# Kernel tuning notes

Measured on AMD Instinct MI355X. Metric: run time of the kernel, lower is better.

The kernel has to match this reference:

```python
import jax, jax.numpy as jnp
import numpy as np

USER_COUNT = 100000
ITEM_COUNT = 100000
DIM = 64
B = 1024
NPOS = 10
NTOP = 50
CLAMP = 40.0
EPS = 1e-05


def setup_inputs() -> dict:
    key = jax.random.key(0)
    k1, k2, k3, k4, k5 = jax.random.split(key, 5)
    user_emb = jax.random.normal(k1, (USER_COUNT, DIM), dtype=jnp.float32) * 0.01
    item_emb = jax.random.normal(k2, (ITEM_COUNT, DIM), dtype=jnp.float32) * 0.01
    batch_user = jax.random.randint(k3, (B,), 0, USER_COUNT)
    pos_items = jax.random.randint(k4, (B, NPOS), 0, ITEM_COUNT)
    top_items = jax.random.randint(k5, (B, NTOP), 0, ITEM_COUNT)
    batch_user_mask = jnp.zeros((B, ITEM_COUNT), dtype=jnp.float32)
    return {
        "user_emb": user_emb,
        "item_emb": item_emb,
        "batch_user": batch_user,
        "pos_items": pos_items,
        "top_items": top_items,
        "batch_user_mask": batch_user_mask,
        "is_final": 1,
    }


def _overall_loss(mat, pos_items, top_items, mask):
    # tops: scores at pos+top indices, [B, NPOS+NTOP]
    tops = jnp.take_along_axis(mat, jnp.concatenate([pos_items, top_items], -1), axis=1)
    tops_els = (jnp.exp(mat) * (1.0 - mask)).sum(1, keepdims=True)  # [B,1]
    els = tops_els - jnp.exp(jnp.take_along_axis(mat, top_items, axis=1)).sum(1, keepdims=True)
    above = tops.reshape(-1, 1)
    below = jnp.broadcast_to(els, (els.shape[0], tops.shape[1])).reshape(-1, 1) + jnp.exp(above)
    below = jnp.log(jnp.clip(below, EPS))
    return -(above - below).sum()


def _rank_loss(mat, pos_items, top_items, mask):
    S_pos = jnp.take_along_axis(mat, pos_items, axis=1)                       # [B,NPOS]
    S_top = jnp.take_along_axis(mat, top_items[:, : NTOP // 2], axis=1)       # [B,NTOP/2]
    exp_masked_sum = (jnp.exp(mat) * (1.0 - mask)).sum(1, keepdims=True)      # [B,1]
    below2 = exp_masked_sum - jnp.exp(S_top).sum(1, keepdims=True)
    above_pos = S_pos.sum(1, keepdims=True)
    above_top = S_top.sum(1, keepdims=True)
    below_pos = jnp.cumsum(jnp.exp(jnp.flip(S_pos, -1)), axis=1)
    below_top = jnp.cumsum(jnp.exp(jnp.flip(S_top, -1)), axis=1)
    below_pos = jnp.log(jnp.clip(below_pos + below2, EPS)).sum(1, keepdims=True)
    below_top = jnp.log(jnp.clip(below_top + below2, EPS)).sum(1, keepdims=True)
    pos_KD_loss = -(above_pos - below_pos).sum()
    S_top_sub = jnp.take_along_axis(mat, top_items[:, : NTOP // 10], axis=1)  # [B,NTOP/10]
    below2_sub = exp_masked_sum - jnp.exp(S_top_sub).sum(1, keepdims=True)
    above_top_sub = S_top_sub.sum(1, keepdims=True)
    below_top_sub = jnp.cumsum(jnp.exp(jnp.flip(S_top_sub, -1)), axis=1)
    below_top_sub = jnp.log(jnp.clip(below_top_sub + below2_sub, EPS)).sum(1, keepdims=True)
    top_KD_loss = -(above_top - below_top).sum() - (above_top_sub - below_top_sub).sum()
    return pos_KD_loss + top_KD_loss / 2


def reference(user_emb, item_emb, batch_user, pos_items, top_items, batch_user_mask, is_final):
    u = user_emb[batch_user]                                  # [B, DIM]
    mat = jnp.clip(u @ item_emb.T, -CLAMP, CLAMP)             # [B, ITEM_COUNT]
    if is_final:
        return _rank_loss(mat, pos_items, top_items, batch_user_mask)
    return _overall_loss(mat, pos_items, top_items, batch_user_mask)
```

## Files before the change

kernel.cpp:

```cpp
#include <hip/hip_runtime.h>
#include <cstddef>
#include <cstdint>

#define USER_COUNT_C 100000
#define ITEM_COUNT_C 100000
#define DIM_C 64
#define B_C 1024
#define NPOS_C 10
#define NTOP_C 50
#define CLAMP_C 40.0f
#define EPS_C 1e-5f

#define NGROUPS 6250
#define NCHUNKS 3125
#define GX 48
#define GY 16

using bf16x8 = __attribute__((ext_vector_type(8))) short;
using f32x4  = __attribute__((ext_vector_type(4))) float;

__global__ void zero_ws_kernel(float* __restrict__ ws) {
    ws[threadIdx.x] = 0.0f;
}

__device__ inline short f2bf(float x) {
    uint32_t b = __float_as_uint(x);
    uint32_t r = (b + 0x7fffu + ((b >> 16) & 1u)) >> 16;
    return (short)r;
}

__device__ inline bf16x8 cvt8(const float* __restrict__ p) {
    float4 v0 = *(const float4*)p;
    float4 v1 = *(const float4*)(p + 4);
    bf16x8 r;
    r[0] = f2bf(v0.x); r[1] = f2bf(v0.y); r[2] = f2bf(v0.z); r[3] = f2bf(v0.w);
    r[4] = f2bf(v1.x); r[5] = f2bf(v1.y); r[6] = f2bf(v1.z); r[7] = f2bf(v1.w);
    return r;
}

__global__ __launch_bounds__(256) void prep_items_kernel(
    const float* __restrict__ item_emb, short* __restrict__ item_bf16) {
    const int t = blockIdx.x * 256 + threadIdx.x;
    const int n16 = t & 15;
    const int q   = (t >> 4) & 3;
    const int h   = (t >> 6) & 1;
    const int g   = t >> 7;
    const int i   = g * 16 + n16;
    bf16x8 v = cvt8(item_emb + (size_t)i * DIM_C + h * 32 + q * 8);
    *(bf16x8*)(item_bf16 + (((size_t)g * 2 + h) * 4 + q) * 128 + n16 * 8) = v;
}

__global__ __launch_bounds__(256, 3) void expsum_mfma5_kernel(
    const float* __restrict__ user_emb,
    const short* __restrict__ item_bf16,
    const int*   __restrict__ batch_user,
    const float* __restrict__ mask,
    float*       __restrict__ exp_sum)
{
    const int tid  = threadIdx.x;
    const int wave = tid >> 6;
    const int lane = tid & 63;
    const int n16  = lane & 15;
    const int quad = lane >> 4;
    const int uBase = blockIdx.y * 64;

    bf16x8 b0[4], b1[4];
    #pragma unroll
    for (int j = 0; j < 4; ++j) {
        const int uidx = batch_user[uBase + j * 16 + n16];
        const float* us = user_emb + (size_t)uidx * DIM_C + quad * 8;
        b0[j] = cvt8(us);
        b1[j] = cvt8(us + 32);
    }

    const float* mbase = mask + (size_t)(uBase + n16) * ITEM_COUNT_C;
    const short* fbase = item_bf16 + quad * 128 + n16 * 8;

    const int c0 = (int)(((long)blockIdx.x * NCHUNKS) / GX);
    const int c1 = (int)(((long)(blockIdx.x + 1) * NCHUNKS) / GX);

    float accE[4] = {0.f, 0.f, 0.f, 0.f};

    for (int c = c0 + wave; c < c1; c += 4) {
        float4 m[4][2];
        #pragma unroll
        for (int j = 0; j < 4; ++j)
            #pragma unroll
            for (int ig = 0; ig < 2; ++ig)
                m[j][ig] = *(const float4*)(mbase + (size_t)j * 16 * ITEM_COUNT_C
                                            + c * 32 + ig * 16 + quad * 4);

        const short* fp = fbase + (size_t)c * 2048;
        const bf16x8 a00 = *(const bf16x8*)fp;
        const bf16x8 a01 = *(const bf16x8*)(fp + 512);
        const bf16x8 a10 = *(const bf16x8*)(fp + 1024);
        const bf16x8 a11 = *(const bf16x8*)(fp + 1536);

        f32x4 acc[2][4];
        #pragma unroll
        for (int j = 0; j < 4; ++j) {
            acc[0][j] = (f32x4){0.f, 0.f, 0.f, 0.f};
            acc[0][j] = __builtin_amdgcn_mfma_f32_16x16x32_bf16(a00, b0[j], acc[0][j], 0, 0, 0);
            acc[0][j] = __builtin_amdgcn_mfma_f32_16x16x32_bf16(a01, b1[j], acc[0][j], 0, 0, 0);
            acc[1][j] = (f32x4){0.f, 0.f, 0.f, 0.f};
            acc[1][j] = __builtin_amdgcn_mfma_f32_16x16x32_bf16(a10, b0[j], acc[1][j], 0, 0, 0);
            acc[1][j] = __builtin_amdgcn_mfma_f32_16x16x32_bf16(a11, b1[j], acc[1][j], 0, 0, 0);
        }

        #pragma unroll
        for (int j = 0; j < 4; ++j)
            #pragma unroll
            for (int ig = 0; ig < 2; ++ig) {
                const float* mp = (const float*)&m[j][ig];
                #pragma unroll
                for (int r = 0; r < 4; ++r) {
                    const float sc = fminf(fmaxf(acc[ig][j][r], -CLAMP_C), CLAMP_C);
                    accE[j] += __expf(sc) * (1.0f - mp[r]);
                }
            }
    }

    #pragma unroll
    for (int j = 0; j < 4; ++j) {
        accE[j] += __shfl_xor(accE[j], 16, 64);
        accE[j] += __shfl_xor(accE[j], 32, 64);
    }
    if (quad == 0) {
        #pragma unroll
        for (int j = 0; j < 4; ++j)
            atomicAdd(&exp_sum[uBase + j * 16 + n16], accE[j]);
    }
}

__global__ __launch_bounds__(256) void expsum_fallback_kernel(
    const float* __restrict__ user_emb,
    const float* __restrict__ item_emb,
    const int*   __restrict__ batch_user,
    const float* __restrict__ mask,
    float*       __restrict__ exp_sum)
{
    const int tid  = threadIdx.x;
    const int wave = tid >> 6;
    const int lane = tid & 63;
    const int n16  = lane & 15;
    const int quad = lane >> 4;
    const int rowBase = blockIdx.y * 64 + wave * 16;

    const int uidx = batch_user[rowBase + n16];
    const float* usrc = user_emb + (size_t)uidx * DIM_C + quad * 8;
    const bf16x8 a0 = cvt8(usrc);
    const bf16x8 a1 = cvt8(usrc + 32);

    float accExp[4] = {0.f, 0.f, 0.f, 0.f};

    for (int t = blockIdx.x; t < NGROUPS / 4; t += 64) {
        const int ibase = t * 64;
        bf16x8 b0[4], b1[4];
        #pragma unroll
        for (int s = 0; s < 4; ++s) {
            const int gi = ibase + s * 16 + n16;
            const float* isrc = item_emb + (size_t)gi * DIM_C + quad * 8;
            b0[s] = cvt8(isrc);
            b1[s] = cvt8(isrc + 32);
        }
        f32x4 acc[4];
        #pragma unroll
        for (int s = 0; s < 4; ++s) {
            acc[s] = (f32x4){0.f, 0.f, 0.f, 0.f};
            acc[s] = __builtin_amdgcn_mfma_f32_16x16x32_bf16(a0, b0[s], acc[s], 0, 0, 0);
            acc[s] = __builtin_amdgcn_mfma_f32_16x16x32_bf16(a1, b1[s], acc[s], 0, 0, 0);
        }
        #pragma unroll
        for (int s = 0; s < 4; ++s)
            #pragma unroll
            for (int reg = 0; reg < 4; ++reg) {
                const int row = rowBase + quad * 4 + reg;
                const float sc = fminf(fmaxf(acc[s][reg], -CLAMP_C), CLAMP_C);
                const float w = 1.0f - mask[(size_t)row * ITEM_COUNT_C + ibase + s * 16 + n16];
                accExp[reg] += __expf(sc) * w;
            }
    }
    #pragma unroll
    for (int off = 1; off < 16; off <<= 1)
        #pragma unroll
        for (int reg = 0; reg < 4; ++reg)
            accExp[reg] += __shfl_xor(accExp[reg], off, 64);
    if (n16 == 0)
        #pragma unroll
        for (int reg = 0; reg < 4; ++reg)
            atomicAdd(&exp_sum[rowBase + quad * 4 + reg], accExp[reg]);
}

__global__ void finalize_kernel(
    const float* __restrict__ user_emb,
    const float* __restrict__ item_emb,
    const int*   __restrict__ batch_user,
    const int*   __restrict__ pos_items,
    const int*   __restrict__ top_items,
    const float* __restrict__ exp_sum,
    const int*   __restrict__ is_final,
    float*       __restrict__ row_loss)
{
    __shared__ float ush[DIM_C];
    __shared__ float s_sh[NPOS_C + NTOP_C];
    const int b = blockIdx.x;
    const int tid = threadIdx.x;
    const int uidx = batch_user[b];
    if (tid < 16)
        *(float4*)&ush[tid * 4] = *(const float4*)(user_emb + (size_t)uidx * DIM_C + tid * 4);
    __syncthreads();

    if (tid < NPOS_C + NTOP_C) {
        const int idx = (tid < NPOS_C) ? pos_items[b * NPOS_C + tid]
                                       : top_items[b * NTOP_C + (tid - NPOS_C)];
        const float* iv = item_emb + (size_t)idx * DIM_C;
        float s = 0.f;
        #pragma unroll
        for (int d4 = 0; d4 < 16; ++d4) {
            const float4 a = *(const float4*)(iv + d4 * 4);
            s += a.x * ush[d4 * 4 + 0] + a.y * ush[d4 * 4 + 1]
               + a.z * ush[d4 * 4 + 2] + a.w * ush[d4 * 4 + 3];
        }
        s_sh[tid] = fminf(fmaxf(s, -CLAMP_C), CLAMP_C);
    }
    __syncthreads();

    if (tid == 0) {
        const float E = exp_sum[b];
        float L;
        if (is_final[0] != 0) {
            float sumExpTop = 0.f, above_top = 0.f;
            for (int i = 0; i < NTOP_C / 2; ++i) {
                const float v = s_sh[NPOS_C + i];
                sumExpTop += __expf(v); above_top += v;
            }
            const float below2 = E - sumExpTop;
            float above_pos = 0.f;
            for (int i = 0; i < NPOS_C; ++i) above_pos += s_sh[i];
            float c = 0.f, below_pos = 0.f;
            for (int i = 0; i < NPOS_C; ++i) {
                c += __expf(s_sh[NPOS_C - 1 - i]);
                below_pos += __logf(fmaxf(c + below2, EPS_C));
            }
            float c2 = 0.f, below_top = 0.f;
            for (int i = 0; i < NTOP_C / 2; ++i) {
                c2 += __expf(s_sh[NPOS_C + NTOP_C / 2 - 1 - i]);
                below_top += __logf(fmaxf(c2 + below2, EPS_C));
            }
            const float pos_KD = below_pos - above_pos;
            float sumExpSub = 0.f, above_sub = 0.f;
            for (int i = 0; i < NTOP_C / 10; ++i) {
                const float v = s_sh[NPOS_C + i];
                sumExpSub += __expf(v); above_sub += v;
            }
            const float below2s = E - sumExpSub;
            float c3 = 0.f, below_sub = 0.f;
            for (int i = 0; i < NTOP_C / 10; ++i) {
                c3 += __expf(s_sh[NPOS_C + NTOP_C / 10 - 1 - i]);
                below_sub += __logf(fmaxf(c3 + below2s, EPS_C));
            }
            const float top_KD = (below_top - above_top) + (below_sub - above_sub);
            L = pos_KD + 0.5f * top_KD;
        } else {
            float sumExpTop = 0.f;
            for (int i = 0; i < NTOP_C; ++i) sumExpTop += __expf(s_sh[NPOS_C + i]);
            const float els = E - sumExpTop;
            L = 0.f;
            for (int j = 0; j < NPOS_C + NTOP_C; ++j) {
                const float a = s_sh[j];
                L += __logf(fmaxf(els + __expf(a), EPS_C)) - a;
            }
        }
        row_loss[b] = L;
    }
}

__global__ void reduce_kernel(const float* __restrict__ rl, float* __restrict__ out) {
    __shared__ float part[16];
    const int tid = threadIdx.x;
    float v = rl[tid];
    #pragma unroll
    for (int off = 32; off > 0; off >>= 1) v += __shfl_down(v, off, 64);
    if ((tid & 63) == 0) part[tid >> 6] = v;
    __syncthreads();
    if (tid == 0) {
        float s = 0.f;
        #pragma unroll
        for (int i = 0; i < 16; ++i) s += part[i];
        out[0] = s;
    }
}

extern "C" void kernel_launch(void* const* d_in, const int* in_sizes, int n_in,
                              void* d_out, int out_size, void* d_ws, size_t ws_size,
                              hipStream_t stream) {
    const float* user_emb   = (const float*)d_in[0];
    const float* item_emb   = (const float*)d_in[1];
    const int*   batch_user = (const int*)d_in[2];
    const int*   pos_items  = (const int*)d_in[3];
    const int*   top_items  = (const int*)d_in[4];
    const float* mask       = (const float*)d_in[5];
    const int*   is_final   = (const int*)d_in[6];
    float* out = (float*)d_out;

    float* exp_sum  = (float*)d_ws;
    float* row_loss = exp_sum + B_C;
    short* item_bf16 = (short*)(row_loss + B_C);
    const size_t need = 2 * B_C * sizeof(float)
                      + (size_t)NGROUPS * 1024 * sizeof(short);

    hipLaunchKernelGGL(zero_ws_kernel, dim3(1), dim3(B_C), 0, stream, exp_sum);
    if (ws_size >= need) {
        hipLaunchKernelGGL(prep_items_kernel, dim3(NGROUPS * 128 / 256), dim3(256),
                           0, stream, item_emb, item_bf16);
        hipLaunchKernelGGL(expsum_mfma5_kernel, dim3(GX, GY), dim3(256),
                           0, stream, user_emb, item_bf16, batch_user, mask, exp_sum);
    } else {
        hipLaunchKernelGGL(expsum_fallback_kernel, dim3(64, B_C / 64), dim3(256),
                           0, stream, user_emb, item_emb, batch_user, mask, exp_sum);
    }
    hipLaunchKernelGGL(finalize_kernel, dim3(B_C), dim3(64), 0, stream,
                       user_emb, item_emb, batch_user, pos_items, top_items,
                       exp_sum, is_final, row_loss);
    hipLaunchKernelGGL(reduce_kernel, dim3(1), dim3(B_C), 0, stream, row_loss, out);
}
```

Before: 593.2 us.

## Split expsum kernel into mask-loader and MFMA waves via LDS double buffer

```diff
diff --git a/kernel.cpp b/kernel.cpp
--- a/kernel.cpp
+++ b/kernel.cpp
@@ -12,9 +12,12 @@
 #define EPS_C 1e-5f
 
 #define NGROUPS 6250
-#define NCHUNKS 3125
+#define TI_T 64
+#define NTILES_T 1563
 #define GX 48
 #define GY 16
+
+#define BAR() asm volatile("s_waitcnt lgkmcnt(0)\n\ts_barrier" ::: "memory")
 
 using bf16x8 = __attribute__((ext_vector_type(8))) short;
 using f32x4  = __attribute__((ext_vector_type(4))) float;
@@ -39,96 +42,136 @@
 }
 
 __global__ __launch_bounds__(256) void prep_items_kernel(
-    const float* __restrict__ item_emb, short* __restrict__ item_bf16) {
+    const float* __restrict__ item_emb, short* __restrict__ item_bf16,
+    float* __restrict__ exp_sum) {
     const int t = blockIdx.x * 256 + threadIdx.x;
+    if (blockIdx.x < 4) exp_sum[blockIdx.x * 256 + threadIdx.x] = 0.0f;
     const int n16 = t & 15;
     const int q   = (t >> 4) & 3;
     const int h   = (t >> 6) & 1;
     const int g   = t >> 7;
     const int i   = g * 16 + n16;
     bf16x8 v = cvt8(item_emb + (size_t)i * DIM_C + h * 32 + q * 8);
-    *(bf16x8*)(item_bf16 + (((size_t)g * 2 + h) * 4 + q) * 128 + n16 * 8) = v;
-}
-
-__global__ __launch_bounds__(256, 3) void expsum_mfma5_kernel(
+    *(bf16x8*)(item_bf16 + (size_t)g * 1024 + h * 512 + q * 128 + n16 * 8) = v;
+}
+
+__global__ __launch_bounds__(256, 3) void expsum_pc_kernel(
     const float* __restrict__ user_emb,
     const short* __restrict__ item_bf16,
     const int*   __restrict__ batch_user,
     const float* __restrict__ mask,
     float*       __restrict__ exp_sum)
 {
+    __shared__ float4 fr[2][1024];
+
     const int tid  = threadIdx.x;
     const int wave = tid >> 6;
     const int lane = tid & 63;
-    const int n16  = lane & 15;
-    const int quad = lane >> 4;
     const int uBase = blockIdx.y * 64;
-
-    bf16x8 b0[4], b1[4];
-    #pragma unroll
-    for (int j = 0; j < 4; ++j) {
-        const int uidx = batch_user[uBase + j * 16 + n16];
-        const float* us = user_emb + (size_t)uidx * DIM_C + quad * 8;
-        b0[j] = cvt8(us);
-        b1[j] = cvt8(us + 32);
-    }
-
-    const float* mbase = mask + (size_t)(uBase + n16) * ITEM_COUNT_C;
-    const short* fbase = item_bf16 + quad * 128 + n16 * 8;
-
-    const int c0 = (int)(((long)blockIdx.x * NCHUNKS) / GX);
-    const int c1 = (int)(((long)(blockIdx.x + 1) * NCHUNKS) / GX);
-
-    float accE[4] = {0.f, 0.f, 0.f, 0.f};
-
-    for (int c = c0 + wave; c < c1; c += 4) {
-        float4 m[4][2];
-        #pragma unroll
-        for (int j = 0; j < 4; ++j)
-            #pragma unroll
-            for (int ig = 0; ig < 2; ++ig)
-                m[j][ig] = *(const float4*)(mbase + (size_t)j * 16 * ITEM_COUNT_C
-                                            + c * 32 + ig * 16 + quad * 4);
-
-        const short* fp = fbase + (size_t)c * 2048;
-        const bf16x8 a00 = *(const bf16x8*)fp;
-        const bf16x8 a01 = *(const bf16x8*)(fp + 512);
-        const bf16x8 a10 = *(const bf16x8*)(fp + 1024);
-        const bf16x8 a11 = *(const bf16x8*)(fp + 1536);
-
-        f32x4 acc[2][4];
+    const int T_blk = (NTILES_T - blockIdx.x + GX - 1) / GX;
+
+    if (wave < 2) {
+        const int plane = wave * 64 + lane;
+        const int r     = plane >> 1;
+        const int half  = plane & 1;
+        const int j     = r >> 4;
+        const int n16   = r & 15;
+        const float* mrow = mask + (size_t)(uBase + r) * ITEM_COUNT_C;
+
+        float4 regA[8], regB[8];
+        auto issue = [&](int k, float4* reg) {
+            if (k >= T_blk) return;
+            const int C = (blockIdx.x + k * GX) * TI_T;
+            #pragma unroll
+            for (int f = 0; f < 8; ++f) {
+                const int col = C + half * 32 + f * 4;
+                const int cc  = col < (ITEM_COUNT_C - 4) ? col : (ITEM_COUNT_C - 4);
+                reg[f] = *(const float4*)(mrow + cc);
+            }
+        };
+
+        issue(0, regA);
+        issue(1, regB);
+        for (int k = 0; k < T_blk; ++k) {
+            float4* reg = (k & 1) ? regB : regA;
+            const int C = (blockIdx.x + k * GX) * TI_T;
+            float4* buf = fr[k & 1];
+            #pragma unroll
+            for (int f = 0; f < 8; ++f) {
+                const int o   = half * 32 + f * 4;
+                const int col = C + o;
+                float4 v = reg[f];
+                if (col >= ITEM_COUNT_C) v = make_float4(1.f, 1.f, 1.f, 1.f);
+                const int s = o >> 4, quad = (o >> 2) & 3;
+                buf[(s * 4 + j) * 64 + quad * 16 + n16] = v;
+            }
+            issue(k + 2, reg);
+            BAR();
+        }
+    } else {
+        const int n16  = lane & 15;
+        const int quad = lane >> 4;
+        const int cw   = wave - 2;
+
+        bf16x8 b0[4], b1[4];
         #pragma unroll
         for (int j = 0; j < 4; ++j) {
-            acc[0][j] = (f32x4){0.f, 0.f, 0.f, 0.f};
-            acc[0][j] = __builtin_amdgcn_mfma_f32_16x16x32_bf16(a00, b0[j], acc[0][j], 0, 0, 0);
-            acc[0][j] = __builtin_amdgcn_mfma_f32_16x16x32_bf16(a01, b1[j], acc[0][j], 0, 0, 0);
-            acc[1][j] = (f32x4){0.f, 0.f, 0.f, 0.f};
-            acc[1][j] = __builtin_amdgcn_mfma_f32_16x16x32_bf16(a10, b0[j], acc[1][j], 0, 0, 0);
-            acc[1][j] = __builtin_amdgcn_mfma_f32_16x16x32_bf16(a11, b1[j], acc[1][j], 0, 0, 0);
-        }
-
-        #pragma unroll
-        for (int j = 0; j < 4; ++j)
-            #pragma unroll
-            for (int ig = 0; ig < 2; ++ig) {
-                const float* mp = (const float*)&m[j][ig];
+            const int uidx = batch_user[uBase + j * 16 + n16];
+            const float* us = user_emb + (size_t)uidx * DIM_C + quad * 8;
+            b0[j] = cvt8(us);
+            b1[j] = cvt8(us + 32);
+        }
+        const short* fbase = item_bf16 + quad * 128 + n16 * 8;
+
+        float accE[4] = {0.f, 0.f, 0.f, 0.f};
+
+        for (int k = 0; k < T_blk; ++k) {
+            const int tile = blockIdx.x + k * GX;
+            const short* fp = fbase + (size_t)(tile * 4 + cw * 2) * 1024;
+            const bf16x8 a00 = *(const bf16x8*)fp;
+            const bf16x8 a01 = *(const bf16x8*)(fp + 512);
+            const bf16x8 a10 = *(const bf16x8*)(fp + 1024);
+            const bf16x8 a11 = *(const bf16x8*)(fp + 1536);
+
+            BAR();
+            const float4* buf = fr[k & 1];
+
+            f32x4 acc0[4], acc1[4];
+            #pragma unroll
+            for (int j = 0; j < 4; ++j) {
+                acc0[j] = (f32x4){0.f, 0.f, 0.f, 0.f};
+                acc0[j] = __builtin_amdgcn_mfma_f32_16x16x32_bf16(a00, b0[j], acc0[j], 0, 0, 0);
+                acc0[j] = __builtin_amdgcn_mfma_f32_16x16x32_bf16(a01, b1[j], acc0[j], 0, 0, 0);
+                acc1[j] = (f32x4){0.f, 0.f, 0.f, 0.f};
+                acc1[j] = __builtin_amdgcn_mfma_f32_16x16x32_bf16(a10, b0[j], acc1[j], 0, 0, 0);
+                acc1[j] = __builtin_amdgcn_mfma_f32_16x16x32_bf16(a11, b1[j], acc1[j], 0, 0, 0);
+            }
+            #pragma unroll
+            for (int j = 0; j < 4; ++j) {
+                const float4 m0 = buf[((cw * 2 + 0) * 4 + j) * 64 + lane];
+                const float4 m1 = buf[((cw * 2 + 1) * 4 + j) * 64 + lane];
+                const float* m0p = (const float*)&m0;
+                const float* m1p = (const float*)&m1;
                 #pragma unroll
                 for (int r = 0; r < 4; ++r) {
-                    const float sc = fminf(fmaxf(acc[ig][j][r], -CLAMP_C), CLAMP_C);
-                    accE[j] += __expf(sc) * (1.0f - mp[r]);
+                    const float s0 = fminf(fmaxf(acc0[j][r], -CLAMP_C), CLAMP_C);
+                    accE[j] += __expf(s0) * (1.0f - m0p[r]);
+                    const float s1 = fminf(fmaxf(acc1[j][r], -CLAMP_C), CLAMP_C);
+                    accE[j] += __expf(s1) * (1.0f - m1p[r]);
                 }
             }
-    }
-
-    #pragma unroll
-    for (int j = 0; j < 4; ++j) {
-        accE[j] += __shfl_xor(accE[j], 16, 64);
-        accE[j] += __shfl_xor(accE[j], 32, 64);
-    }
-    if (quad == 0) {
-        #pragma unroll
-        for (int j = 0; j < 4; ++j)
-            atomicAdd(&exp_sum[uBase + j * 16 + n16], accE[j]);
+        }
+
+        #pragma unroll
+        for (int j = 0; j < 4; ++j) {
+            accE[j] += __shfl_xor(accE[j], 16, 64);
+            accE[j] += __shfl_xor(accE[j], 32, 64);
+        }
+        if (quad == 0) {
+            #pragma unroll
+            for (int j = 0; j < 4; ++j)
+                atomicAdd(&exp_sum[uBase + j * 16 + n16], accE[j]);
+        }
     }
 }
 
@@ -307,15 +350,15 @@
     float* row_loss = exp_sum + B_C;
     short* item_bf16 = (short*)(row_loss + B_C);
     const size_t need = 2 * B_C * sizeof(float)
-                      + (size_t)NGROUPS * 1024 * sizeof(short);
-
-    hipLaunchKernelGGL(zero_ws_kernel, dim3(1), dim3(B_C), 0, stream, exp_sum);
+                      + ((size_t)NGROUPS + 16) * 1024 * sizeof(short);
+
     if (ws_size >= need) {
         hipLaunchKernelGGL(prep_items_kernel, dim3(NGROUPS * 128 / 256), dim3(256),
-                           0, stream, item_emb, item_bf16);
-        hipLaunchKernelGGL(expsum_mfma5_kernel, dim3(GX, GY), dim3(256),
+                           0, stream, item_emb, item_bf16, exp_sum);
+        hipLaunchKernelGGL(expsum_pc_kernel, dim3(GX, GY), dim3(256),
                            0, stream, user_emb, item_bf16, batch_user, mask, exp_sum);
     } else {
+        hipLaunchKernelGGL(zero_ws_kernel, dim3(1), dim3(B_C), 0, stream, exp_sum);
         hipLaunchKernelGGL(expsum_fallback_kernel, dim3(64, B_C / 64), dim3(256),
                            0, stream, user_emb, item_emb, batch_user, mask, exp_sum);
     }
```

After: 695.7 us. 17.3% more time.
